# Kernel optimization log

Hardware: AMD Instinct MI355X
Metric: run time of the kernel (lower is better)

The kernel has to match this reference:

```python
import jax, jax.numpy as jnp
import numpy as np

N, E = 50000, 800000
IN, HID, OUT, T = 96, 128, 64, 8
THETA = 0.5


def setup_inputs() -> dict:
    key = jax.random.key(0)
    ks = jax.random.split(key, 8)
    x = jax.random.normal(ks[0], (N, IN), dtype=jnp.float32)
    edge_weight = jax.random.uniform(ks[1], (E,), dtype=jnp.float32)
    W1 = jax.random.normal(ks[2], (IN, HID), dtype=jnp.float32) * (2.0 / np.sqrt(IN + HID))
    W2 = jax.random.normal(ks[3], (HID, OUT), dtype=jnp.float32) * (2.0 / np.sqrt(HID + OUT))
    # Bernoulli(1 - theta) masks, fixed per MC sample (created in __init__)
    mask1 = (jax.random.uniform(ks[4], (T, IN, HID)) < (1.0 - THETA)).astype(jnp.float32)
    mask2 = (jax.random.uniform(ks[5], (T, HID, OUT)) < (1.0 - THETA)).astype(jnp.float32)
    src = jax.random.randint(ks[6], (E,), 0, N, dtype=jnp.int32)
    dst = jax.random.randint(ks[7], (E,), 0, N, dtype=jnp.int32)
    return {"x": x, "edge_weight": edge_weight, "W1": W1, "W2": W2,
            "mask1": mask1, "mask2": mask2, "src": src, "dst": dst}


def _spmm(feat, edge_weight, src, dst, n_nodes):
    # u_mul_e('feat','edge_weight') followed by fn.sum onto dst nodes
    msg = feat[src] * edge_weight[:, None]          # [E, D]
    return jax.ops.segment_sum(msg, dst, num_segments=n_nodes)  # [N, D]


def reference(x, edge_weight, W1, W2, mask1, mask2, src, dst):
    n = x.shape[0]
    # first aggregation is mask-independent -> compute once, share across T samples
    agg1 = _spmm(x, edge_weight, src, dst, n)       # [N, IN]

    def per_sample(m1, m2):
        h = jax.nn.relu(agg1 @ (W1 * m1))           # [N, HID]
        agg2 = _spmm(h, edge_weight, src, dst, n)   # [N, HID]
        return agg2 @ (W2 * m2)                     # [N, OUT]

    # stack of the T per-sample outputs (torch version returns a list)
    return jax.vmap(per_sample)(mask1, mask2)       # [T, N, OUT]
```

## Files before the change

kernel.cpp:

```cpp
#include <hip/hip_runtime.h>

#define N_NODES 50000
#define N_EDGES 800000
#define IN_F 96
#define HID_F 128
#define OUT_F 64
#define T_S 8
#define CAP 48

#define NB_XB 4688
#define NB_WPREP 640
#define NB_INIT (NB_XB + NB_WPREP)

typedef __attribute__((ext_vector_type(8))) short short8;
typedef __attribute__((ext_vector_type(4))) float float4v;
typedef __attribute__((ext_vector_type(2))) unsigned uint2v;
typedef __attribute__((ext_vector_type(4))) unsigned uint4v;

__device__ __forceinline__ float bf2f(unsigned short h) {
    unsigned u = ((unsigned)h) << 16;
    float f;
    __builtin_memcpy(&f, &u, 4);
    return f;
}
__device__ __forceinline__ unsigned short f2bf(float f) {
    unsigned u;
    __builtin_memcpy(&u, &f, 4);
    unsigned r = (u + 0x7fffu + ((u >> 16) & 1u)) >> 16;
    return (unsigned short)r;
}
__device__ __forceinline__ float bf_lo(unsigned u) {
    unsigned v = u << 16;
    float f;
    __builtin_memcpy(&f, &v, 4);
    return f;
}
__device__ __forceinline__ float bf_hi(unsigned u) {
    unsigned v = u & 0xffff0000u;
    float f;
    __builtin_memcpy(&f, &v, 4);
    return f;
}

__global__ __launch_bounds__(256) void k_init(const float* __restrict__ x,
                                              unsigned short* __restrict__ xb,
                                              const float* __restrict__ W1,
                                              const float* __restrict__ W2,
                                              const float* __restrict__ m1,
                                              const float* __restrict__ m2,
                                              unsigned short* __restrict__ wf) {
    int bid = blockIdx.x;
    if (bid < NB_XB) {
        int i = bid * 256 + threadIdx.x;
        int idx = i * 4;
        if (idx < N_NODES * IN_F) {
            float4v v = __builtin_nontemporal_load((const float4v*)(x + idx));
            uint2v r;
            r.x = (unsigned)f2bf(v.x) | ((unsigned)f2bf(v.y) << 16);
            r.y = (unsigned)f2bf(v.z) | ((unsigned)f2bf(v.w) << 16);
            *(uint2v*)(xb + idx) = r;
        }
        return;
    }
    bid -= NB_XB;
    {
        int gid = bid * 256 + threadIdx.x;
        if (gid >= T_S * 20480) return;
        int t = gid / 20480;
        int idx = gid % 20480;
        float val;
        if (idx < 12288) {
            int j = idx & 7, lane = (idx >> 3) & 63, fr = idx >> 9;
            int kk = fr >> 3, nt = fr & 7;
            int k = kk * 32 + (lane >> 4) * 8 + j;
            int n = nt * 16 + (lane & 15);
            val = W1[k * HID_F + n] * m1[((size_t)t * IN_F + k) * HID_F + n];
        } else {
            int i2 = idx - 12288;
            int j = i2 & 7, lane = (i2 >> 3) & 63, fr = i2 >> 9;
            int kk = fr >> 2, ot = fr & 3;
            int k = kk * 32 + (lane >> 4) * 8 + j;
            int o = ot * 16 + (lane & 15);
            val = W2[k * OUT_F + o] * m2[((size_t)t * HID_F + k) * OUT_F + o];
        }
        wf[gid] = f2bf(val);
    }
}

__global__ void k_fillB(const int* __restrict__ src, const int* __restrict__ dst,
                        const float* __restrict__ ew, int* __restrict__ cursor,
                        uint2v* __restrict__ bucket) {
    int e = blockIdx.x * 256 + threadIdx.x;
    if (e < N_EDGES) {
        int d = dst[e];
        int pos = atomicAdd(&cursor[d], 1);
        if (pos < CAP) {
            uint2v c;
            c.x = (unsigned)src[e];
            c.y = __float_as_uint(ew[e]);
            __builtin_nontemporal_store(c, &bucket[(size_t)d * CAP + pos]);
        }
    }
}

__global__ __launch_bounds__(256) void k_spmm1(const unsigned short* __restrict__ xb,
                                               const int* __restrict__ cursor,
                                               const uint2v* __restrict__ bucket,
                                               unsigned short* __restrict__ agg1) {
    int wave = threadIdx.x >> 6, lane = threadIdx.x & 63;
    int node = blockIdx.x * 4 + wave;
    if (lane >= 48) return;
    int cnt = cursor[node];
    if (cnt > CAP) cnt = CAP;
    int beg = node * CAP, end = beg + cnt;
    const unsigned* xrow = (const unsigned*)xb;
    float a0 = 0.f, a1 = 0.f;
    int e = beg;
    for (; e + 7 < end; e += 8) {
        uint2v c[8];
        unsigned d[8];
#pragma unroll
        for (int i = 0; i < 8; i++) c[i] = bucket[e + i];
#pragma unroll
        for (int i = 0; i < 8; i++) d[i] = xrow[(size_t)c[i].x * 48 + lane];
#pragma unroll
        for (int i = 0; i < 8; i++) {
            float wv = __uint_as_float(c[i].y);
            a0 = fmaf(wv, bf_lo(d[i]), a0);
            a1 = fmaf(wv, bf_hi(d[i]), a1);
        }
    }
    for (; e + 3 < end; e += 4) {
        uint2v c[4];
        unsigned d[4];
#pragma unroll
        for (int i = 0; i < 4; i++) c[i] = bucket[e + i];
#pragma unroll
        for (int i = 0; i < 4; i++) d[i] = xrow[(size_t)c[i].x * 48 + lane];
#pragma unroll
        for (int i = 0; i < 4; i++) {
            float wv = __uint_as_float(c[i].y);
            a0 = fmaf(wv, bf_lo(d[i]), a0);
            a1 = fmaf(wv, bf_hi(d[i]), a1);
        }
    }
    for (; e < end; e++) {
        uint2v c = bucket[e];
        float wv = __uint_as_float(c.y);
        unsigned d = xrow[(size_t)c.x * 48 + lane];
        a0 = fmaf(wv, bf_lo(d), a0);
        a1 = fmaf(wv, bf_hi(d), a1);
    }
    ((unsigned*)agg1)[(size_t)node * 48 + lane] =
        (unsigned)f2bf(a0) | ((unsigned)f2bf(a1) << 16);
}

__global__ __launch_bounds__(256) void k_gemm(const unsigned short* __restrict__ agg1,
                                              const unsigned short* __restrict__ wfrags,
                                              unsigned short* __restrict__ P, int tBase,
                                              int nodeStride, int tMul) {
    __shared__ __align__(16) unsigned short ldsW[20480];
    __shared__ __align__(16) unsigned short ldsH[4][2176];
    int t = tBase + blockIdx.y;
    const uint4* wsrc = (const uint4*)(wfrags + (size_t)t * 20480);
    uint4* wdst = (uint4*)ldsW;
    for (int i = threadIdx.x; i < 2560; i += 256) wdst[i] = wsrc[i];
    __syncthreads();

    int wave = threadIdx.x >> 6, lane = threadIdx.x & 63;
    int quad = lane >> 4, l15 = lane & 15;

    for (int it = 0; it < 8; it++) {
        int node = blockIdx.x * 512 + it * 64 + wave * 16 + l15;
        bool v = node < N_NODES;

        short8 a[3];
        if (v) {
            const unsigned short* ap = agg1 + (size_t)node * IN_F;
            a[0] = *(const short8*)(ap + 0 * 32 + quad * 8);
            a[1] = *(const short8*)(ap + 1 * 32 + quad * 8);
            a[2] = *(const short8*)(ap + 2 * 32 + quad * 8);
        } else {
            short8 z = {0, 0, 0, 0, 0, 0, 0, 0};
            a[0] = z; a[1] = z; a[2] = z;
        }

        for (int nt = 0; nt < 8; nt++) {
            float4v acc = {0.f, 0.f, 0.f, 0.f};
            for (int kk = 0; kk < 3; kk++) {
                short8 w = *(const short8*)&ldsW[(kk * 8 + nt) * 512 + lane * 8];
                acc = __builtin_amdgcn_mfma_f32_16x16x32_bf16(w, a[kk], acc, 0, 0, 0);
            }
            unsigned h0 = f2bf(fmaxf(acc[0], 0.f));
            unsigned h1 = f2bf(fmaxf(acc[1], 0.f));
            unsigned h2 = f2bf(fmaxf(acc[2], 0.f));
            unsigned h3 = f2bf(fmaxf(acc[3], 0.f));
            uint2 pk;
            pk.x = h0 | (h1 << 16);
            pk.y = h2 | (h3 << 16);
            *(uint2*)&ldsH[wave][l15 * 136 + nt * 16 + quad * 4] = pk;
        }

        short8 hf[4];
        for (int kk = 0; kk < 4; kk++)
            hf[kk] = *(const short8*)&ldsH[wave][l15 * 136 + kk * 32 + quad * 8];

        unsigned short* Pt = P + (size_t)node * nodeStride + (size_t)t * tMul;
        for (int ot = 0; ot < 4; ot++) {
            float4v acc = {0.f, 0.f, 0.f, 0.f};
            for (int kk = 0; kk < 4; kk++) {
                short8 w = *(const short8*)&ldsW[12288 + (kk * 4 + ot) * 512 + lane * 8];
                acc = __builtin_amdgcn_mfma_f32_16x16x32_bf16(w, hf[kk], acc, 0, 0, 0);
            }
            if (v) {
                uint2 pk;
                pk.x = (unsigned)f2bf(acc[0]) | ((unsigned)f2bf(acc[1]) << 16);
                pk.y = (unsigned)f2bf(acc[2]) | ((unsigned)f2bf(acc[3]) << 16);
                *(uint2*)(Pt + ot * 16 + quad * 4) = pk;
            }
        }
    }
}

__global__ __launch_bounds__(256) void k_spmm2(const unsigned short* __restrict__ P,
                                               const int* __restrict__ cursor,
                                               const uint2v* __restrict__ bucket,
                                               float* __restrict__ out) {
    int wave = threadIdx.x >> 6, lane = threadIdx.x & 63;
    int node = blockIdx.x * 4 + wave;
    int cnt = cursor[node];
    if (cnt > CAP) cnt = CAP;
    int beg = node * CAP, end = beg + cnt;
    const uint4v* Pl = (const uint4v*)P + lane;
    float acc[8] = {0.f, 0.f, 0.f, 0.f, 0.f, 0.f, 0.f, 0.f};
    int e = beg;
    for (; e + 7 < end; e += 8) {
        uint2v c[8];
        uint4v d[8];
#pragma unroll
        for (int i = 0; i < 8; i++) c[i] = bucket[e + i];
#pragma unroll
        for (int i = 0; i < 8; i++) d[i] = Pl[(size_t)c[i].x * 64];
#pragma unroll
        for (int i = 0; i < 8; i++) {
            float wv = __uint_as_float(c[i].y);
            acc[0] = fmaf(wv, bf_lo(d[i].x), acc[0]);
            acc[1] = fmaf(wv, bf_hi(d[i].x), acc[1]);
            acc[2] = fmaf(wv, bf_lo(d[i].y), acc[2]);
            acc[3] = fmaf(wv, bf_hi(d[i].y), acc[3]);
            acc[4] = fmaf(wv, bf_lo(d[i].z), acc[4]);
            acc[5] = fmaf(wv, bf_hi(d[i].z), acc[5]);
            acc[6] = fmaf(wv, bf_lo(d[i].w), acc[6]);
            acc[7] = fmaf(wv, bf_hi(d[i].w), acc[7]);
        }
    }
    for (; e + 3 < end; e += 4) {
        uint2v c[4];
        uint4v d[4];
#pragma unroll
        for (int i = 0; i < 4; i++) c[i] = bucket[e + i];
#pragma unroll
        for (int i = 0; i < 4; i++) d[i] = Pl[(size_t)c[i].x * 64];
#pragma unroll
        for (int i = 0; i < 4; i++) {
            float wv = __uint_as_float(c[i].y);
            acc[0] = fmaf(wv, bf_lo(d[i].x), acc[0]);
            acc[1] = fmaf(wv, bf_hi(d[i].x), acc[1]);
            acc[2] = fmaf(wv, bf_lo(d[i].y), acc[2]);
            acc[3] = fmaf(wv, bf_hi(d[i].y), acc[3]);
            acc[4] = fmaf(wv, bf_lo(d[i].z), acc[4]);
            acc[5] = fmaf(wv, bf_hi(d[i].z), acc[5]);
            acc[6] = fmaf(wv, bf_lo(d[i].w), acc[6]);
            acc[7] = fmaf(wv, bf_hi(d[i].w), acc[7]);
        }
    }
    for (; e < end; e++) {
        uint2v c = bucket[e];
        float wv = __uint_as_float(c.y);
        uint4v d = Pl[(size_t)c.x * 64];
        acc[0] = fmaf(wv, bf_lo(d.x), acc[0]);
        acc[1] = fmaf(wv, bf_hi(d.x), acc[1]);
        acc[2] = fmaf(wv, bf_lo(d.y), acc[2]);
        acc[3] = fmaf(wv, bf_hi(d.y), acc[3]);
        acc[4] = fmaf(wv, bf_lo(d.z), acc[4]);
        acc[5] = fmaf(wv, bf_hi(d.z), acc[5]);
        acc[6] = fmaf(wv, bf_lo(d.w), acc[6]);
        acc[7] = fmaf(wv, bf_hi(d.w), acc[7]);
    }
    int t = lane >> 3, o = (lane & 7) * 8;
    float* op = out + ((size_t)t * N_NODES + node) * OUT_F + o;
    float4v v0 = {acc[0], acc[1], acc[2], acc[3]};
    float4v v1 = {acc[4], acc[5], acc[6], acc[7]};
    *(float4v*)op = v0;
    *(float4v*)(op + 4) = v1;
}

__global__ __launch_bounds__(512) void k_spmm2_1t(const unsigned short* __restrict__ P,
                                                  const int* __restrict__ cursor,
                                                  const uint2v* __restrict__ bucket,
                                                  float* __restrict__ out) {
    int node = blockIdx.x * 8 + (threadIdx.x >> 6);
    int o = threadIdx.x & 63;
    if (node >= N_NODES) return;
    int cnt = cursor[node];
    if (cnt > CAP) cnt = CAP;
    int beg = node * CAP, end = beg + cnt;
    const unsigned short* Pt = P + o;
    float a0 = 0.f, a1 = 0.f, a2 = 0.f, a3 = 0.f;
    int e = beg;
    for (; e + 3 < end; e += 4) {
        uint2v c0 = bucket[e];
        uint2v c1 = bucket[e + 1];
        uint2v c2 = bucket[e + 2];
        uint2v c3 = bucket[e + 3];
        a0 += __uint_as_float(c0.y) * bf2f(Pt[(size_t)c0.x * OUT_F]);
        a1 += __uint_as_float(c1.y) * bf2f(Pt[(size_t)c1.x * OUT_F]);
        a2 += __uint_as_float(c2.y) * bf2f(Pt[(size_t)c2.x * OUT_F]);
        a3 += __uint_as_float(c3.y) * bf2f(Pt[(size_t)c3.x * OUT_F]);
    }
    for (; e < end; e++) {
        uint2v c = bucket[e];
        a0 += __uint_as_float(c.y) * bf2f(Pt[(size_t)c.x * OUT_F]);
    }
    out[(size_t)node * OUT_F + o] = a0 + a1 + a2 + a3;
}

extern "C" void kernel_launch(void* const* d_in, const int* in_sizes, int n_in,
                              void* d_out, int out_size, void* d_ws, size_t ws_size,
                              hipStream_t stream) {
    const float* x = (const float*)d_in[0];
    const float* ew = (const float*)d_in[1];
    const float* W1 = (const float*)d_in[2];
    const float* W2 = (const float*)d_in[3];
    const float* m1 = (const float*)d_in[4];
    const float* m2 = (const float*)d_in[5];
    const int* src = (const int*)d_in[6];
    const int* dst = (const int*)d_in[7];
    float* out = (float*)d_out;

    char* w = (char*)d_ws;
    size_t off = 0;
    auto alloc = [&](size_t bytes) -> void* {
        void* p = (void*)(w + off);
        off += (bytes + 255) & ~(size_t)255;
        return p;
    };
    int* cursor = (int*)alloc((size_t)N_NODES * 4);
    uint2v* bucket = (uint2v*)alloc((size_t)N_NODES * CAP * 8);
    unsigned short* agg1 = (unsigned short*)alloc((size_t)N_NODES * IN_F * 2);
    unsigned short* wf = (unsigned short*)alloc((size_t)T_S * 20480 * 2);

    size_t unionBase = off;
    size_t pBytesBatched = (size_t)T_S * N_NODES * OUT_F * 2;
    size_t xbBytes = (size_t)N_NODES * IN_F * 2;
    bool batched = ws_size >= unionBase + (pBytesBatched > xbBytes ? pBytesBatched : xbBytes);
    unsigned short* xb = (unsigned short*)(w + unionBase);
    unsigned short* P = (unsigned short*)(w + unionBase);
    if (!batched) {
        xb = (unsigned short*)(w + unionBase);
        P = (unsigned short*)(w + unionBase + ((xbBytes + 255) & ~(size_t)255));
    }

    hipMemsetAsync(cursor, 0, (size_t)N_NODES * 4, stream);
    k_init<<<NB_INIT, 256, 0, stream>>>(x, xb, W1, W2, m1, m2, wf);
    k_fillB<<<N_EDGES / 256, 256, 0, stream>>>(src, dst, ew, cursor, bucket);
    k_spmm1<<<N_NODES / 4, 256, 0, stream>>>(xb, cursor, bucket, agg1);

    if (batched) {
        k_gemm<<<dim3(98, 8), 256, 0, stream>>>(agg1, wf, P, 0, T_S * OUT_F, OUT_F);
        k_spmm2<<<N_NODES / 4, 256, 0, stream>>>(P, cursor, bucket, out);
    } else {
        for (int t = 0; t < T_S; t++) {
            k_gemm<<<dim3(98, 1), 256, 0, stream>>>(agg1, wf, P, t, OUT_F, 0);
            k_spmm2_1t<<<6250, 512, 0, stream>>>(P, cursor, bucket,
                                                 out + (size_t)t * N_NODES * OUT_F);
        }
    }
}
```

Measured before the change: 367.0 us.

## Fold cursor memset into prep kernel and vectorize spmm1 with 16-byte gathers

```diff
diff --git a/kernel.cpp b/kernel.cpp
--- a/kernel.cpp
+++ b/kernel.cpp
@@ -8,9 +8,10 @@
 #define T_S 8
 #define CAP 48
 
+#define NB_ZERO 196
 #define NB_XB 4688
 #define NB_WPREP 640
-#define NB_INIT (NB_XB + NB_WPREP)
+#define NB_PREP (NB_ZERO + NB_XB + NB_WPREP)
 
 typedef __attribute__((ext_vector_type(8))) short short8;
 typedef __attribute__((ext_vector_type(4))) float float4v;
@@ -42,7 +43,8 @@
     return f;
 }
 
-__global__ __launch_bounds__(256) void k_init(const float* __restrict__ x,
+__global__ __launch_bounds__(256) void k_prep(int* __restrict__ cursor,
+                                              const float* __restrict__ x,
                                               unsigned short* __restrict__ xb,
                                               const float* __restrict__ W1,
                                               const float* __restrict__ W2,
@@ -50,6 +52,12 @@
                                               const float* __restrict__ m2,
                                               unsigned short* __restrict__ wf) {
     int bid = blockIdx.x;
+    if (bid < NB_ZERO) {
+        int i = bid * 256 + threadIdx.x;
+        if (i < N_NODES) cursor[i] = 0;
+        return;
+    }
+    bid -= NB_ZERO;
     if (bid < NB_XB) {
         int i = bid * 256 + threadIdx.x;
         int idx = i * 4;
@@ -109,50 +117,62 @@
                                                unsigned short* __restrict__ agg1) {
     int wave = threadIdx.x >> 6, lane = threadIdx.x & 63;
     int node = blockIdx.x * 4 + wave;
-    if (lane >= 48) return;
+    int g = lane >> 4, d = lane & 15;
+    int dd = (d < 12) ? d : 0;
     int cnt = cursor[node];
     if (cnt > CAP) cnt = CAP;
     int beg = node * CAP, end = beg + cnt;
-    const unsigned* xrow = (const unsigned*)xb;
-    float a0 = 0.f, a1 = 0.f;
+    const uint4v* xrow = (const uint4v*)xb;
+    float acc[8] = {0.f, 0.f, 0.f, 0.f, 0.f, 0.f, 0.f, 0.f};
     int e = beg;
-    for (; e + 7 < end; e += 8) {
-        uint2v c[8];
-        unsigned d[8];
-#pragma unroll
-        for (int i = 0; i < 8; i++) c[i] = bucket[e + i];
-#pragma unroll
-        for (int i = 0; i < 8; i++) d[i] = xrow[(size_t)c[i].x * 48 + lane];
-#pragma unroll
-        for (int i = 0; i < 8; i++) {
-            float wv = __uint_as_float(c[i].y);
-            a0 = fmaf(wv, bf_lo(d[i]), a0);
-            a1 = fmaf(wv, bf_hi(d[i]), a1);
-        }
-    }
-    for (; e + 3 < end; e += 4) {
+    for (; e + 15 < end; e += 16) {
         uint2v c[4];
-        unsigned d[4];
-#pragma unroll
-        for (int i = 0; i < 4; i++) c[i] = bucket[e + i];
-#pragma unroll
-        for (int i = 0; i < 4; i++) d[i] = xrow[(size_t)c[i].x * 48 + lane];
+        uint4v dt[4];
+#pragma unroll
+        for (int i = 0; i < 4; i++) c[i] = bucket[e + i * 4 + g];
+#pragma unroll
+        for (int i = 0; i < 4; i++) dt[i] = xrow[(size_t)c[i].x * 12 + dd];
 #pragma unroll
         for (int i = 0; i < 4; i++) {
             float wv = __uint_as_float(c[i].y);
-            a0 = fmaf(wv, bf_lo(d[i]), a0);
-            a1 = fmaf(wv, bf_hi(d[i]), a1);
-        }
-    }
-    for (; e < end; e++) {
-        uint2v c = bucket[e];
-        float wv = __uint_as_float(c.y);
-        unsigned d = xrow[(size_t)c.x * 48 + lane];
-        a0 = fmaf(wv, bf_lo(d), a0);
-        a1 = fmaf(wv, bf_hi(d), a1);
-    }
-    ((unsigned*)agg1)[(size_t)node * 48 + lane] =
-        (unsigned)f2bf(a0) | ((unsigned)f2bf(a1) << 16);
+            acc[0] = fmaf(wv, bf_lo(dt[i].x), acc[0]);
+            acc[1] = fmaf(wv, bf_hi(dt[i].x), acc[1]);
+            acc[2] = fmaf(wv, bf_lo(dt[i].y), acc[2]);
+            acc[3] = fmaf(wv, bf_hi(dt[i].y), acc[3]);
+            acc[4] = fmaf(wv, bf_lo(dt[i].z), acc[4]);
+            acc[5] = fmaf(wv, bf_hi(dt[i].z), acc[5]);
+            acc[6] = fmaf(wv, bf_lo(dt[i].w), acc[6]);
+            acc[7] = fmaf(wv, bf_hi(dt[i].w), acc[7]);
+        }
+    }
+    for (; e < end; e += 4) {
+        int ee = e + g;
+        bool ea = ee < end;
+        uint2v c = bucket[ea ? ee : beg];
+        float wv = ea ? __uint_as_float(c.y) : 0.f;
+        uint4v dt = xrow[(size_t)c.x * 12 + dd];
+        acc[0] = fmaf(wv, bf_lo(dt.x), acc[0]);
+        acc[1] = fmaf(wv, bf_hi(dt.x), acc[1]);
+        acc[2] = fmaf(wv, bf_lo(dt.y), acc[2]);
+        acc[3] = fmaf(wv, bf_hi(dt.y), acc[3]);
+        acc[4] = fmaf(wv, bf_lo(dt.z), acc[4]);
+        acc[5] = fmaf(wv, bf_hi(dt.z), acc[5]);
+        acc[6] = fmaf(wv, bf_lo(dt.w), acc[6]);
+        acc[7] = fmaf(wv, bf_hi(dt.w), acc[7]);
+    }
+#pragma unroll
+    for (int j = 0; j < 8; j++) {
+        acc[j] += __shfl_xor(acc[j], 16);
+        acc[j] += __shfl_xor(acc[j], 32);
+    }
+    if (lane < 12) {
+        uint4v pk;
+        pk.x = (unsigned)f2bf(acc[0]) | ((unsigned)f2bf(acc[1]) << 16);
+        pk.y = (unsigned)f2bf(acc[2]) | ((unsigned)f2bf(acc[3]) << 16);
+        pk.z = (unsigned)f2bf(acc[4]) | ((unsigned)f2bf(acc[5]) << 16);
+        pk.w = (unsigned)f2bf(acc[6]) | ((unsigned)f2bf(acc[7]) << 16);
+        ((uint4v*)agg1)[(size_t)node * 12 + d] = pk;
+    }
 }
 
 __global__ __launch_bounds__(256) void k_gemm(const unsigned short* __restrict__ agg1,
@@ -361,8 +381,7 @@
         P = (unsigned short*)(w + unionBase + ((xbBytes + 255) & ~(size_t)255));
     }
 
-    hipMemsetAsync(cursor, 0, (size_t)N_NODES * 4, stream);
-    k_init<<<NB_INIT, 256, 0, stream>>>(x, xb, W1, W2, m1, m2, wf);
+    k_prep<<<NB_PREP, 256, 0, stream>>>(cursor, x, xb, W1, W2, m1, m2, wf);
     k_fillB<<<N_EDGES / 256, 256, 0, stream>>>(src, dst, ew, cursor, bucket);
     k_spmm1<<<N_NODES / 4, 256, 0, stream>>>(xb, cursor, bucket, agg1);
 
```

After: 362.7 us, median of 2. No clear change (-1.2%).
